# Optimization experiments

Hardware: AMD Instinct MI355X
Metric: run time of the kernel (lower is better)

The kernel has to match this reference:

```python
import jax, jax.numpy as jnp
import numpy as np

B = 256
N = 256


def setup_inputs() -> dict:
    key = jax.random.key(0)
    ks = jax.random.split(key, 6)
    X = jax.random.normal(ks[0], (B, N), dtype=jnp.float32)
    context = jax.random.normal(ks[1], (B, N), dtype=jnp.float32)
    W = jax.random.normal(ks[2], (N, N), dtype=jnp.float32) * 0.1
    scale = jnp.ones((1,), dtype=jnp.float32)
    A = jax.random.uniform(ks[3], (N, N), dtype=jnp.float32)
    cl_weight = jax.random.normal(ks[4], (N * N, N), dtype=jnp.float32) * 0.02
    cl_bias = jax.random.normal(ks[5], (N * N,), dtype=jnp.float32) * 0.02
    t = 3
    return {"X": X, "context": context, "W": W, "scale": scale, "A": A,
            "cl_weight": cl_weight, "cl_bias": cl_bias, "t": t}


def reference(X, context, W, scale, A, cl_weight, cl_bias, t):
    # context_L path: context-conditioned adjustment of W, shape [B, N, N]
    Bsz, n = X.shape
    adjust = (context @ cl_weight.T + cl_bias).reshape(Bsz, n, n)
    W_new = adjust + W  # broadcast [N,N] over batch
    # diag term: sum over rows i of (W_new @ A)[b, i, k] = einsum bij,jk->bk
    d = jnp.einsum('bij,jk->bk', W_new, A)
    eye = jnp.eye(n, dtype=X.dtype)
    L = d[:, :, None] * eye - W_new          # diag_embed(d) - W_new, [B,N,N]
    new_context = context * (t / (t + 1)) + X / (t + 1)
    L_T = scale * jnp.swapaxes(L, -1, -2)    # [B,N,N]
    update = jnp.einsum('bn,bnm->bm', X, L_T)  # matmul(X[...,None,:], L_T).squeeze()
    return (update, new_context)
```

## Files before the change

kernel.cpp:

```cpp
#include <hip/hip_runtime.h>

#define N 256
#define NN 65536

typedef __attribute__((ext_vector_type(8))) __bf16 bf16x8;
typedef __attribute__((ext_vector_type(4))) __bf16 bf16x4v;
typedef __attribute__((ext_vector_type(4))) float f32x4;

#define F_PART   0u
#define F_CSPART 2097152u
#define F_WSC    2621440u
#define F_CSB    2621696u
#define F_SFULL  2654464u
#define F_YADJ   2720000u
#define WS_FLOATS 2785536u

static __device__ __forceinline__ f32x4 mfma16(bf16x8 a, bf16x8 b, f32x4 c) {
  return __builtin_amdgcn_mfma_f32_16x16x32_bf16(a, b, c, 0, 0, 0);
}
static __device__ __forceinline__ bf16x4v pack4(float4 v) {
  bf16x4v r;
  r[0] = (__bf16)v.x; r[1] = (__bf16)v.y; r[2] = (__bf16)v.z; r[3] = (__bf16)v.w;
  return r;
}
static __device__ __forceinline__ bf16x8 pack8(float4 a, float4 b) {
  bf16x8 r;
  r[0] = (__bf16)a.x; r[1] = (__bf16)a.y; r[2] = (__bf16)a.z; r[3] = (__bf16)a.w;
  r[4] = (__bf16)b.x; r[5] = (__bf16)b.y; r[6] = (__bf16)b.z; r[7] = (__bf16)b.w;
  return r;
}

#define BARL()                                                            \
  asm volatile("s_waitcnt lgkmcnt(0)" ::: "memory");                      \
  __builtin_amdgcn_s_barrier();                                           \
  __builtin_amdgcn_sched_barrier(0);

__global__ void __launch_bounds__(256) kbig(
    const float* __restrict__ X, const float* __restrict__ ctx,
    const float* __restrict__ W, const float* __restrict__ clb,
    const float* __restrict__ clw, float* __restrict__ ws)
{
  extern __shared__ char smem[];
  float* csl = (float*)(smem + 32768);
  float* xl  = (float*)(smem + 40960);
  float* red = (float*)smem;
  const int t = threadIdx.x;
  const int bh = blockIdx.x >> 8;
  const int rem = blockIdx.x & 255;
  const int mt = rem >> 5, s = rem & 31;
  const int n0 = s * 8, m0g = mt * 32, b0g = bh * 64;

  const int lane = t & 63, w = t >> 6;
  const int wb = w * 16;
  const int l15 = lane & 15, lhi = lane >> 4;
  const int swz = (l15 & 7) << 4;
  const float4* clwf4 = (const float4*)clw;

  bf16x8 af[8];
#pragma unroll
  for (int c = 0; c < 8; ++c) {
    const float4* p = (const float4*)(ctx + (b0g + wb + l15) * N +
                                      c * 32 + lhi * 8);
    af[c] = pack8(p[0], p[1]);
  }
  if (t < 64) {
    const float4* xp = (const float4*)(X + (b0g + t) * N + n0);
    const float4 x0 = xp[0], x1 = xp[1];
    xl[0 * 64 + t] = x0.x; xl[1 * 64 + t] = x0.y;
    xl[2 * 64 + t] = x0.z; xl[3 * 64 + t] = x0.w;
    xl[4 * 64 + t] = x1.x; xl[5 * 64 + t] = x1.y;
    xl[6 * 64 + t] = x1.z; xl[7 * 64 + t] = x1.w;
  }

  const f32x4 zero = {0.f, 0.f, 0.f, 0.f};
  f32x4 acc[2];
  acc[0] = zero; acc[1] = zero;

#define STAGE(TT)                                                           \
  {                                                                         \
    float4 r[8];                                                            \
    _Pragma("unroll")                                                       \
    for (int i = 0; i < 8; ++i) {                                           \
      const int rowl = w * 8 + i;                                           \
      r[i] = clwf4[(size_t)((m0g + rowl) * 256 + n0 + (TT)) * 64 + lane];   \
    }                                                                       \
    _Pragma("unroll")                                                       \
    for (int i = 0; i < 8; ++i) {                                           \
      const int rowl = w * 8 + i;                                           \
      *(bf16x4v*)(smem + ((TT) & 1) * 16384 + rowl * 512 +                  \
                  ((lane * 8) ^ ((rowl & 7) << 4))) = pack4(r[i]);          \
    }                                                                       \
    if (bh == 0) {                                                          \
      float4 cso = r[0];                                                    \
      _Pragma("unroll")                                                     \
      for (int i = 1; i < 8; ++i) {                                         \
        cso.x += r[i].x; cso.y += r[i].y;                                   \
        cso.z += r[i].z; cso.w += r[i].w;                                   \
      }                                                                     \
      *(float4*)(csl + ((TT) & 1) * 1024 + w * 256 + lane * 4) = cso;       \
    }                                                                       \
    BARL();                                                                 \
  }

#define COMP(NNV)                                                           \
  {                                                                         \
    const char* buf = smem + ((NNV) & 1) * 16384;                           \
    f32x4 h[2];                                                             \
    h[0] = zero; h[1] = zero;                                               \
    _Pragma("unroll")                                                       \
    for (int c = 0; c < 8; ++c) {                                           \
      const int kb = c * 64 + lhi * 16;                                     \
      bf16x8 b0 = *(const bf16x8*)(buf + l15 * 512 + (kb ^ swz));           \
      bf16x8 b1 = *(const bf16x8*)(buf + (16 + l15) * 512 + (kb ^ swz));    \
      h[0] = mfma16(af[c], b0, h[0]);                                       \
      h[1] = mfma16(af[c], b1, h[1]);                                       \
    }                                                                       \
    _Pragma("unroll")                                                       \
    for (int r = 0; r < 4; ++r) {                                           \
      const float xv = xl[(NNV) * 64 + wb + lhi * 4 + r];                   \
      acc[0][r] += xv * h[0][r];                                            \
      acc[1][r] += xv * h[1][r];                                            \
    }                                                                       \
    if (bh == 0) {                                                          \
      const int cb = ((NNV) & 1) * 1024;                                    \
      float cv = csl[cb + t] + csl[cb + 256 + t] +                          \
                 csl[cb + 512 + t] + csl[cb + 768 + t];                     \
      ws[F_CSPART + mt * 65536u + (n0 + (NNV)) * 256 + t] = cv;             \
    }                                                                       \
  }

  STAGE(0) COMP(0)
  STAGE(1) COMP(1)
  STAGE(2) COMP(2)
  STAGE(3) COMP(3)
  STAGE(4) COMP(4)
  STAGE(5) COMP(5)
  STAGE(6) COMP(6)
  STAGE(7) COMP(7)
#undef STAGE
#undef COMP

  const int base = blockIdx.x * 2048;
#pragma unroll
  for (int fm = 0; fm < 2; ++fm)
#pragma unroll
    for (int r = 0; r < 4; ++r)
      ws[F_PART + base + (wb + lhi * 4 + r) * 32 + fm * 16 + l15] =
          acc[fm][r];

  if (mt == 0 && bh == 0) {
    __syncthreads();
    const float4* wp = (const float4*)(W + t * N + s * 8);
    const float4* cp = (const float4*)(clb + t * N + s * 8);
    const float4 a0 = wp[0], a1 = wp[1], c0 = cp[0], c1 = cp[1];
    red[0 * 256 + t] = a0.x + c0.x; red[1 * 256 + t] = a0.y + c0.y;
    red[2 * 256 + t] = a0.z + c0.z; red[3 * 256 + t] = a0.w + c0.w;
    red[4 * 256 + t] = a1.x + c1.x; red[5 * 256 + t] = a1.y + c1.y;
    red[6 * 256 + t] = a1.z + c1.z; red[7 * 256 + t] = a1.w + c1.w;
    __syncthreads();
    if (t < 64) {
      const int jj = t >> 3, seg = t & 7;
      float v = 0.f;
#pragma unroll
      for (int i = 0; i < 32; ++i) v += red[jj * 256 + seg * 32 + i];
      v += __shfl_xor(v, 1);
      v += __shfl_xor(v, 2);
      v += __shfl_xor(v, 4);
      if (seg == 0) ws[F_WSC + s * 8 + jj] = v;
    }
  }
}

__global__ void __launch_bounds__(256) kred(float* __restrict__ ws)
{
  const int o = blockIdx.x * 256 + threadIdx.x;
  const int b = o >> 8, col = o & 255;
  const int mt = col >> 5, ml = col & 31;
  const int bhh = b >> 6, bl = b & 63;
  float y = 0.f;
#pragma unroll
  for (int si = 0; si < 32; ++si)
    y += ws[F_PART + (size_t)(bhh * 256 + mt * 32 + si) * 2048 + bl * 32 + ml];
  ws[F_YADJ + o] = y;
  float cv = 0.f;
#pragma unroll
  for (int q = 0; q < 8; ++q)
    cv += ws[F_CSPART + q * 65536u + o];
  ((__bf16*)(ws + F_CSB))[o] = (__bf16)cv;
}

__global__ void __launch_bounds__(256) kred2(
    const float* __restrict__ ctx, float* __restrict__ ws)
{
  const int t = threadIdx.x, blk = blockIdx.x;
  const int b0 = (blk >> 3) * 32, j0 = (blk & 7) * 32;
  const int lane = t & 63, w = t >> 6;
  const int l15 = lane & 15, lhi = lane >> 4;
  const int wqb = (w >> 1) * 16, wqj = (w & 1) * 16;
  const char* csb = (const char*)(ws + F_CSB);

  f32x4 accq = {0.f, 0.f, 0.f, 0.f};
#pragma unroll
  for (int c = 0; c < 8; ++c) {
    const float4* p = (const float4*)(ctx + (b0 + wqb + l15) * N +
                                      c * 32 + lhi * 8);
    bf16x8 a = pack8(p[0], p[1]);
    bf16x8 b = *(const bf16x8*)(csb + (j0 + wqj + l15) * 512 +
                                c * 64 + lhi * 16);
    accq = mfma16(a, b, accq);
  }
  const int j = j0 + wqj + l15;
  const float wscv = ws[F_WSC + j];
#pragma unroll
  for (int r = 0; r < 4; ++r) {
    const int b = b0 + wqb + lhi * 4 + r;
    ws[F_SFULL + b * N + j] = accq[r] + wscv;
  }
}

__global__ void __launch_bounds__(256) kfin(
    const float* __restrict__ X, const float* __restrict__ ctx,
    const float* __restrict__ W, const float* __restrict__ clb,
    const float* __restrict__ A, const float* __restrict__ scale,
    const int* __restrict__ tptr, float* __restrict__ out,
    float* __restrict__ ws)
{
  extern __shared__ char smem[];
  const int t = threadIdx.x, blk = blockIdx.x;
  const int b0 = (blk >> 3) * 32, k0 = (blk & 7) * 32;
  {
    const int row = t >> 3, q = t & 7;
    const int sw = (row & 7) << 4;
    const float4* sp = (const float4*)(ws + F_SFULL + (b0 + row) * N);
    const float4* xp = (const float4*)(X + (b0 + row) * N);
    const float4* wp = (const float4*)(W + (k0 + row) * N);
    const float4* cp = (const float4*)(clb + (k0 + row) * N);
#pragma unroll
    for (int i = 0; i < 8; ++i) {
      const int f4 = q * 8 + i;
      const int off = row * 512 + ((f4 * 8) ^ sw);
      *(bf16x4v*)(smem + off) = pack4(sp[f4]);
      *(bf16x4v*)(smem + 16384 + off) = pack4(xp[f4]);
      const float4 wv = wp[f4], cv = cp[f4];
      float4 s2;
      s2.x = wv.x + cv.x; s2.y = wv.y + cv.y;
      s2.z = wv.z + cv.z; s2.w = wv.w + cv.w;
      *(bf16x4v*)(smem + 49152 + off) = pack4(s2);
    }
    const float4* ap = (const float4*)(A + t * N + k0);
    char* at = smem + 32768;
#pragma unroll
    for (int i = 0; i < 8; ++i) {
      const float4 v = ap[i];
      const int kk = i * 4;
      *(__bf16*)(at + (kk + 0) * 512 + ((t * 2) ^ (((kk + 0) & 7) << 4))) = (__bf16)v.x;
      *(__bf16*)(at + (kk + 1) * 512 + ((t * 2) ^ (((kk + 1) & 7) << 4))) = (__bf16)v.y;
      *(__bf16*)(at + (kk + 2) * 512 + ((t * 2) ^ (((kk + 2) & 7) << 4))) = (__bf16)v.z;
      *(__bf16*)(at + (kk + 3) * 512 + ((t * 2) ^ (((kk + 3) & 7) << 4))) = (__bf16)v.w;
    }
  }
  __syncthreads();
  const int lane = t & 63, w = t >> 6;
  const int l15 = lane & 15, lhi = lane >> 4;
  const int wqb = (w >> 1) * 16, wqk = (w & 1) * 16;
  const int swz = (l15 & 7) << 4;
  f32x4 accd = {0.f, 0.f, 0.f, 0.f}, accw = {0.f, 0.f, 0.f, 0.f};
#pragma unroll
  for (int c = 0; c < 8; ++c) {
    const int kb = c * 64 + lhi * 16;
    bf16x8 as  = *(const bf16x8*)(smem + (wqb + l15) * 512 + (kb ^ swz));
    bf16x8 aat = *(const bf16x8*)(smem + 32768 + (wqk + l15) * 512 + (kb ^ swz));
    bf16x8 ax  = *(const bf16x8*)(smem + 16384 + (wqb + l15) * 512 + (kb ^ swz));
    bf16x8 awc = *(const bf16x8*)(smem + 49152 + (wqk + l15) * 512 + (kb ^ swz));
    accd = mfma16(as, aat, accd);
    accw = mfma16(ax, awc, accw);
  }
  const float sc = scale[0];
  const float tf = (float)(*tptr);
  const float c1 = tf / (tf + 1.f), c2 = 1.f / (tf + 1.f);
#pragma unroll
  for (int r = 0; r < 4; ++r) {
    const int b = b0 + wqb + lhi * 4 + r, k = k0 + wqk + l15;
    const int idx = b * N + k;
    const float xv = X[idx];
    out[idx] = sc * (xv * accd[r] - accw[r] - ws[F_YADJ + idx]);
    out[NN + idx] = ctx[idx] * c1 + xv * c2;
  }
}

extern "C" void kernel_launch(void* const* d_in, const int* in_sizes, int n_in,
                              void* d_out, int out_size, void* d_ws, size_t ws_size,
                              hipStream_t stream)
{
  (void)in_sizes; (void)n_in; (void)out_size;
  const float* X     = (const float*)d_in[0];
  const float* ctx   = (const float*)d_in[1];
  const float* W     = (const float*)d_in[2];
  const float* scale = (const float*)d_in[3];
  const float* A     = (const float*)d_in[4];
  const float* clw   = (const float*)d_in[5];
  const float* clb   = (const float*)d_in[6];
  const int*   tptr  = (const int*)d_in[7];
  float* out = (float*)d_out;
  float* ws  = (float*)d_ws;

  if (ws_size < (size_t)WS_FLOATS * sizeof(float)) return;

  (void)hipFuncSetAttribute((const void*)kbig,
                            hipFuncAttributeMaxDynamicSharedMemorySize, 43008);
  (void)hipFuncSetAttribute((const void*)kfin,
                            hipFuncAttributeMaxDynamicSharedMemorySize, 65536);

  kbig<<<1024, 256, 43008, stream>>>(X, ctx, W, clb, clw, ws);
  kred<<<256, 256, 0, stream>>>(ws);
  kred2<<<64, 256, 0, stream>>>(ctx, ws);
  kfin<<<64, 256, 65536, stream>>>(X, ctx, W, clb, A, scale, tptr, out, ws);
}
```

Baseline: 54.77 us.

## Split kbig n-range across four times more blocks with smaller shared memory

Each kbig block now handles 2 n-slices instead of 8, so the grid grows from 1024 to 4096 blocks. Shared memory drops to a single 16 KB buffer, and X values are read straight into registers instead of being staged in LDS. The aim is more parallelism and occupancy for the memory-bound stream over cl_weight (256 MB of fp32). In exchange, the partial-sum buffer grows fourfold and kred now reduces 128 partials per output instead of 32, which adds workspace traffic. The ctx A-fragment loads are also repeated across four times as many blocks.

Measured after the change: 76.99 us. 40.6% more time.

```diff
diff --git a/kernel.cpp b/kernel.cpp
--- a/kernel.cpp
+++ b/kernel.cpp
@@ -8,12 +8,12 @@
 typedef __attribute__((ext_vector_type(4))) float f32x4;
 
 #define F_PART   0u
-#define F_CSPART 2097152u
-#define F_WSC    2621440u
-#define F_CSB    2621696u
-#define F_SFULL  2654464u
-#define F_YADJ   2720000u
-#define WS_FLOATS 2785536u
+#define F_CSPART 8388608u
+#define F_WSC    8912896u
+#define F_CSB    8913152u
+#define F_SFULL  8945920u
+#define F_YADJ   9011456u
+#define WS_FLOATS 9076992u
 
 static __device__ __forceinline__ f32x4 mfma16(bf16x8 a, bf16x8 b, f32x4 c) {
   return __builtin_amdgcn_mfma_f32_16x16x32_bf16(a, b, c, 0, 0, 0);
@@ -30,25 +30,21 @@
   return r;
 }
 
-#define BARL()                                                            \
-  asm volatile("s_waitcnt lgkmcnt(0)" ::: "memory");                      \
-  __builtin_amdgcn_s_barrier();                                           \
-  __builtin_amdgcn_sched_barrier(0);
-
 __global__ void __launch_bounds__(256) kbig(
     const float* __restrict__ X, const float* __restrict__ ctx,
     const float* __restrict__ W, const float* __restrict__ clb,
     const float* __restrict__ clw, float* __restrict__ ws)
 {
   extern __shared__ char smem[];
-  float* csl = (float*)(smem + 32768);
-  float* xl  = (float*)(smem + 40960);
+  float* csl = (float*)(smem + 16384);
   float* red = (float*)smem;
   const int t = threadIdx.x;
-  const int bh = blockIdx.x >> 8;
-  const int rem = blockIdx.x & 255;
-  const int mt = rem >> 5, s = rem & 31;
-  const int n0 = s * 8, m0g = mt * 32, b0g = bh * 64;
+  const int blk = blockIdx.x;
+  const int tp = blk & 3;
+  const int s  = (blk >> 2) & 31;
+  const int mt = (blk >> 7) & 7;
+  const int bh = blk >> 10;
+  const int n0 = s * 8 + tp * 2, m0g = mt * 32, b0g = bh * 64;
 
   const int lane = t & 63, w = t >> 6;
   const int wb = w * 16;
@@ -63,14 +59,12 @@
                                       c * 32 + lhi * 8);
     af[c] = pack8(p[0], p[1]);
   }
-  if (t < 64) {
-    const float4* xp = (const float4*)(X + (b0g + t) * N + n0);
-    const float4 x0 = xp[0], x1 = xp[1];
-    xl[0 * 64 + t] = x0.x; xl[1 * 64 + t] = x0.y;
-    xl[2 * 64 + t] = x0.z; xl[3 * 64 + t] = x0.w;
-    xl[4 * 64 + t] = x1.x; xl[5 * 64 + t] = x1.y;
-    xl[6 * 64 + t] = x1.z; xl[7 * 64 + t] = x1.w;
-  }
+  float xrv[2][4];
+#pragma unroll
+  for (int TT = 0; TT < 2; ++TT)
+#pragma unroll
+    for (int r = 0; r < 4; ++r)
+      xrv[TT][r] = X[(b0g + wb + lhi * 4 + r) * N + n0 + TT];
 
   const f32x4 zero = {0.f, 0.f, 0.f, 0.f};
   f32x4 acc[2];
@@ -87,7 +81,7 @@
     _Pragma("unroll")                                                       \
     for (int i = 0; i < 8; ++i) {                                           \
       const int rowl = w * 8 + i;                                           \
-      *(bf16x4v*)(smem + ((TT) & 1) * 16384 + rowl * 512 +                  \
+      *(bf16x4v*)(smem + rowl * 512 +                                       \
                   ((lane * 8) ^ ((rowl & 7) << 4))) = pack4(r[i]);          \
     }                                                                       \
     if (bh == 0) {                                                          \
@@ -97,50 +91,43 @@
         cso.x += r[i].x; cso.y += r[i].y;                                   \
         cso.z += r[i].z; cso.w += r[i].w;                                   \
       }                                                                     \
-      *(float4*)(csl + ((TT) & 1) * 1024 + w * 256 + lane * 4) = cso;       \
-    }                                                                       \
-    BARL();                                                                 \
-  }
-
-#define COMP(NNV)                                                           \
+      *(float4*)(csl + w * 256 + lane * 4) = cso;                           \
+    }                                                                       \
+    __syncthreads();                                                        \
+  }
+
+#define COMP(TT)                                                            \
   {                                                                         \
-    const char* buf = smem + ((NNV) & 1) * 16384;                           \
     f32x4 h[2];                                                             \
     h[0] = zero; h[1] = zero;                                               \
     _Pragma("unroll")                                                       \
     for (int c = 0; c < 8; ++c) {                                           \
       const int kb = c * 64 + lhi * 16;                                     \
-      bf16x8 b0 = *(const bf16x8*)(buf + l15 * 512 + (kb ^ swz));           \
-      bf16x8 b1 = *(const bf16x8*)(buf + (16 + l15) * 512 + (kb ^ swz));    \
+      bf16x8 b0 = *(const bf16x8*)(smem + l15 * 512 + (kb ^ swz));          \
+      bf16x8 b1 = *(const bf16x8*)(smem + (16 + l15) * 512 + (kb ^ swz));   \
       h[0] = mfma16(af[c], b0, h[0]);                                       \
       h[1] = mfma16(af[c], b1, h[1]);                                       \
     }                                                                       \
     _Pragma("unroll")                                                       \
     for (int r = 0; r < 4; ++r) {                                           \
-      const float xv = xl[(NNV) * 64 + wb + lhi * 4 + r];                   \
-      acc[0][r] += xv * h[0][r];                                            \
-      acc[1][r] += xv * h[1][r];                                            \
+      acc[0][r] += xrv[TT][r] * h[0][r];                                    \
+      acc[1][r] += xrv[TT][r] * h[1][r];                                    \
     }                                                                       \
     if (bh == 0) {                                                          \
-      const int cb = ((NNV) & 1) * 1024;                                    \
-      float cv = csl[cb + t] + csl[cb + 256 + t] +                          \
-                 csl[cb + 512 + t] + csl[cb + 768 + t];                     \
-      ws[F_CSPART + mt * 65536u + (n0 + (NNV)) * 256 + t] = cv;             \
-    }                                                                       \
-  }
-
-  STAGE(0) COMP(0)
-  STAGE(1) COMP(1)
-  STAGE(2) COMP(2)
-  STAGE(3) COMP(3)
-  STAGE(4) COMP(4)
-  STAGE(5) COMP(5)
-  STAGE(6) COMP(6)
-  STAGE(7) COMP(7)
+      float cvv = csl[t] + csl[256 + t] + csl[512 + t] + csl[768 + t];      \
+      ws[F_CSPART + mt * 65536u + (size_t)(n0 + (TT)) * 256 + t] = cvv;     \
+    }                                                                       \
+  }
+
+  STAGE(0)
+  COMP(0)
+  __syncthreads();
+  STAGE(1)
+  COMP(1)
 #undef STAGE
 #undef COMP
 
-  const int base = blockIdx.x * 2048;
+  const size_t base = (size_t)blk * 2048;
 #pragma unroll
   for (int fm = 0; fm < 2; ++fm)
 #pragma unroll
@@ -148,7 +135,7 @@
       ws[F_PART + base + (wb + lhi * 4 + r) * 32 + fm * 16 + l15] =
           acc[fm][r];
 
-  if (mt == 0 && bh == 0) {
+  if (mt == 0 && bh == 0 && tp == 0) {
     __syncthreads();
     const float4* wp = (const float4*)(W + t * N + s * 8);
     const float4* cp = (const float4*)(clb + t * N + s * 8);
@@ -175,12 +162,14 @@
 {
   const int o = blockIdx.x * 256 + threadIdx.x;
   const int b = o >> 8, col = o & 255;
-  const int mt = col >> 5, ml = col & 31;
+  const int mtm = col >> 5, ml = col & 31;
   const int bhh = b >> 6, bl = b & 63;
+  const size_t sbase = F_PART + (size_t)(bhh * 1024 + mtm * 128) * 2048 +
+                       bl * 32 + ml;
   float y = 0.f;
-#pragma unroll
-  for (int si = 0; si < 32; ++si)
-    y += ws[F_PART + (size_t)(bhh * 256 + mt * 32 + si) * 2048 + bl * 32 + ml];
+#pragma unroll 16
+  for (int q = 0; q < 128; ++q)
+    y += ws[sbase + (size_t)q * 2048];
   ws[F_YADJ + o] = y;
   float cv = 0.f;
 #pragma unroll
@@ -306,12 +295,10 @@
 
   if (ws_size < (size_t)WS_FLOATS * sizeof(float)) return;
 
-  (void)hipFuncSetAttribute((const void*)kbig,
-                            hipFuncAttributeMaxDynamicSharedMemorySize, 43008);
   (void)hipFuncSetAttribute((const void*)kfin,
                             hipFuncAttributeMaxDynamicSharedMemorySize, 65536);
 
-  kbig<<<1024, 256, 43008, stream>>>(X, ctx, W, clb, clw, ws);
+  kbig<<<4096, 256, 20480, stream>>>(X, ctx, W, clb, clw, ws);
   kred<<<256, 256, 0, stream>>>(ws);
   kred2<<<64, 256, 0, stream>>>(ctx, ws);
   kfin<<<64, 256, 65536, stream>>>(X, ctx, W, clb, A, scale, tptr, out, ws);
```
